# Performance work log

Hardware: AMD Instinct MI355X
Metric: run time of the kernel (lower is better)

Reference implementation:

```python
import jax, jax.numpy as jnp
import numpy as np

N, E, H, C, D_EDGE, G = 50000, 800000, 4, 64, 16, 64
NEG_SLOPE = 0.2  # PyG GATConv default negative_slope
EPS = 1e-5       # GraphNorm eps


def setup_inputs() -> dict:
    key = jax.random.key(0)
    ks = jax.random.split(key, 10)
    node = jax.random.normal(ks[0], (N, C), jnp.float32)
    edge_index = jax.random.randint(ks[1], (2, E), 0, N, dtype=jnp.int32)
    edge_attr = jax.random.normal(ks[2], (E, D_EDGE), jnp.float32)
    batch_ptr = jnp.sort(jax.random.randint(ks[3], (N,), 0, G, dtype=jnp.int32))
    s = 1.0 / np.sqrt(C)
    W = jax.random.normal(ks[4], (C, H * C), jnp.float32) * s
    W_edge = jax.random.normal(ks[5], (D_EDGE, H * C), jnp.float32) / np.sqrt(D_EDGE)
    att_src = jax.random.normal(ks[6], (H, C), jnp.float32) * s
    att_dst = jax.random.normal(ks[7], (H, C), jnp.float32) * s
    att_edge = jax.random.normal(ks[8], (H, C), jnp.float32) * s
    bias = jnp.zeros((C,), jnp.float32)
    gn_weight = jnp.ones((C,), jnp.float32)
    gn_bias = jnp.zeros((C,), jnp.float32)
    gn_scale = jnp.ones((C,), jnp.float32)  # GraphNorm mean_scale
    return dict(node=node, edge_index=edge_index, edge_attr=edge_attr,
                batch_ptr=batch_ptr, W=W, W_edge=W_edge, att_src=att_src,
                att_dst=att_dst, att_edge=att_edge, bias=bias,
                gn_weight=gn_weight, gn_bias=gn_bias, gn_scale=gn_scale)


def reference(node, edge_index, edge_attr, batch_ptr, W, W_edge,
              att_src, att_dst, att_edge, bias, gn_weight, gn_bias, gn_scale):
    src, dst = edge_index[0], edge_index[1]
    # shared src/dst projection (PyG GATConv with int in_channels)
    x = (node @ W).reshape(N, H, C)                      # [N,H,C]
    a_src = (x * att_src).sum(-1)                        # [N,H]
    a_dst = (x * att_dst).sum(-1)                        # [N,H]
    xe = (edge_attr @ W_edge).reshape(E, H, C)           # [E,H,C]
    a_edge = (xe * att_edge).sum(-1)                     # [E,H]
    alpha = a_src[src] + a_dst[dst] + a_edge             # [E,H]
    alpha = jax.nn.leaky_relu(alpha, NEG_SLOPE)
    # segment softmax over incoming edges of each dst node
    amax = jax.ops.segment_max(alpha, dst, num_segments=N)
    amax = jnp.where(jnp.isfinite(amax), amax, 0.0)
    ex = jnp.exp(alpha - amax[dst])
    denom = jax.ops.segment_sum(ex, dst, num_segments=N)
    att = ex / (denom[dst] + 1e-16)                      # [E,H]
    # weighted scatter-add of source features
    msg = x[src] * att[:, :, None]                       # [E,H,C]
    out = jax.ops.segment_sum(msg, dst, num_segments=N)  # [N,H,C]
    out = out.mean(axis=1) + bias                        # concat=False -> head mean
    # GraphNorm(out, batch)
    cnt = jnp.maximum(jax.ops.segment_sum(jnp.ones((N,), out.dtype), batch_ptr,
                                          num_segments=G), 1.0)[:, None]
    mean = jax.ops.segment_sum(out, batch_ptr, num_segments=G) / cnt
    o = out - mean[batch_ptr] * gn_scale
    var = jax.ops.segment_sum(o * o, batch_ptr, num_segments=G) / cnt
    o = o / jnp.sqrt(var + EPS)[batch_ptr]
    y = jax.nn.relu(gn_weight * o + gn_bias)
    return (y, att)
```

## Files before the change

kernel.cpp:

```cpp
#include <hip/hip_runtime.h>
#include <math.h>

#define NN 50000
#define EE 800000
#define HH 4
#define CC 64
#define DE 16
#define GG 64
#define HC 256
#define NEG 0.2f
#define EPSV 1e-5f
#define NB 196
#define SB 16

typedef __attribute__((ext_vector_type(8))) short short8;
typedef __attribute__((ext_vector_type(4))) float f32x4;
typedef __attribute__((ext_vector_type(2))) float f32x2;

__device__ __forceinline__ unsigned short f2bf(float f) {
  unsigned int x = __float_as_uint(f);
  unsigned int r = (x + 0x7fff + ((x >> 16) & 1)) >> 16;
  return (unsigned short)r;
}
__device__ __forceinline__ float lrelu(float a) {
  return fmaxf(a, 0.f) + NEG * fminf(a, 0.f);
}

__global__ __launch_bounds__(256) void k_prep(
    const float* __restrict__ W, const float* __restrict__ We,
    const float* __restrict__ ae_, unsigned short* __restrict__ Wbt,
    float* __restrict__ v_edge, int* __restrict__ hist) {
  int b = blockIdx.x, t = threadIdx.x;
  if (b < 64) {
    Wbt[(size_t)t * 64 + b] = f2bf(W[b * HC + (t & 3) * 64 + (t >> 2)]);
  } else if (b == 64) {
    if (t < DE * HH) {
      int d = t >> 2, h = t & 3;
      float s = 0.f;
      for (int c = 0; c < CC; ++c)
        s += We[d * HC + h * CC + c] * ae_[h * CC + c];
      v_edge[t] = s;
    }
  } else {
    int idx = (b - 65) * 256 + t;
    if (idx < NN) hist[idx] = 0;
  }
}

__global__ __launch_bounds__(256) void k_xproj(
    const float* __restrict__ node, const unsigned short* __restrict__ Wbt,
    const float* __restrict__ att_src, const float* __restrict__ att_dst,
    unsigned short* __restrict__ x16, float* __restrict__ a_src,
    float* __restrict__ a_dst, const int* __restrict__ ei,
    int* __restrict__ hist) {
  {
    int e = blockIdx.x * 256 + threadIdx.x;
    atomicAdd(&hist[ei[EE + e]], 1);
  }
  int lane = threadIdx.x & 63;
  int w = threadIdx.x >> 6;
  int m = lane & 15, quad = lane >> 4;
  int m0 = blockIdx.x * 16;
  __shared__ unsigned short xs[16][260];
  const float* arow = node + (size_t)(m0 + m) * CC + quad * 8;
  float4 af0 = *(const float4*)(arow);
  float4 af1 = *(const float4*)(arow + 4);
  float4 af2 = *(const float4*)(arow + 32);
  float4 af3 = *(const float4*)(arow + 36);
  short8 a0 = {(short)f2bf(af0.x), (short)f2bf(af0.y), (short)f2bf(af0.z),
               (short)f2bf(af0.w), (short)f2bf(af1.x), (short)f2bf(af1.y),
               (short)f2bf(af1.z), (short)f2bf(af1.w)};
  short8 a1 = {(short)f2bf(af2.x), (short)f2bf(af2.y), (short)f2bf(af2.z),
               (short)f2bf(af2.w), (short)f2bf(af3.x), (short)f2bf(af3.y),
               (short)f2bf(af3.z), (short)f2bf(af3.w)};
  float sa[4] = {0, 0, 0, 0}, sd[4] = {0, 0, 0, 0};
#pragma unroll
  for (int i = 0; i < 4; ++i) {
    int t = (w * 4 + i) * 16 + m;
    const unsigned short* bp = Wbt + (size_t)t * 64 + quad * 8;
    short8 b0 = *(const short8*)(bp);
    short8 b1 = *(const short8*)(bp + 32);
    f32x4 acc = {0.f, 0.f, 0.f, 0.f};
    acc = __builtin_amdgcn_mfma_f32_16x16x32_bf16(a0, b0, acc, 0, 0, 0);
    acc = __builtin_amdgcn_mfma_f32_16x16x32_bf16(a1, b1, acc, 0, 0, 0);
    float us_t = att_src[(t & 3) * CC + (t >> 2)];
    float ud_t = att_dst[(t & 3) * CC + (t >> 2)];
#pragma unroll
    for (int r = 0; r < 4; ++r) {
      xs[quad * 4 + r][t] = f2bf(acc[r]);
      sa[r] += acc[r] * us_t;
      sd[r] += acc[r] * ud_t;
    }
  }
  __shared__ float lss[4][16][4], lsd[4][16][4];
#pragma unroll
  for (int r = 0; r < 4; ++r) {
    sa[r] += __shfl_xor(sa[r], 4);
    sa[r] += __shfl_xor(sa[r], 8);
    sd[r] += __shfl_xor(sd[r], 4);
    sd[r] += __shfl_xor(sd[r], 8);
  }
  if ((lane & 12) == 0) {
#pragma unroll
    for (int r = 0; r < 4; ++r) {
      lss[w][quad * 4 + r][lane & 3] = sa[r];
      lsd[w][quad * 4 + r][lane & 3] = sd[r];
    }
  }
  __syncthreads();
  int t = threadIdx.x;
  if (t < 64) {
    int row = t >> 2, h = t & 3;
    a_src[(size_t)(m0 + row) * 4 + h] =
        lss[0][row][h] + lss[1][row][h] + lss[2][row][h] + lss[3][row][h];
    a_dst[(size_t)(m0 + row) * 4 + h] =
        lsd[0][row][h] + lsd[1][row][h] + lsd[2][row][h] + lsd[3][row][h];
  }
  {
    int row = t >> 4, seg = t & 15;
    const unsigned short* xr = &xs[0][0] + row * 260 + seg * 16;
    uint2 lo = *(const uint2*)(xr);
    uint2 hi = *(const uint2*)(xr + 4);
    uint4 o;
    o.x = lo.x; o.y = lo.y; o.z = hi.x; o.w = hi.y;
    uint4* xg = (uint4*)(x16 + (size_t)m0 * HC);
    xg[row * 32 + seg * 2] = o;
    uint2 lo2 = *(const uint2*)(xr + 8);
    uint2 hi2 = *(const uint2*)(xr + 12);
    uint4 o2;
    o2.x = lo2.x; o2.y = lo2.y; o2.z = hi2.x; o2.w = hi2.y;
    xg[row * 32 + seg * 2 + 1] = o2;
  }
}

__global__ __launch_bounds__(256) void k_scanA(
    const int* __restrict__ hist, int* __restrict__ bsum) {
  __shared__ int s[256];
  int t = threadIdx.x;
  int idx = blockIdx.x * 256 + t;
  s[t] = (idx < NN) ? hist[idx] : 0;
  __syncthreads();
  for (int d = 128; d; d >>= 1) {
    if (t < d) s[t] += s[t + d];
    __syncthreads();
  }
  if (t == 0) bsum[blockIdx.x] = s[0];
}

__global__ __launch_bounds__(256) void k_scanC(
    const int* __restrict__ hist, const int* __restrict__ bsum,
    int* __restrict__ ptr, int* __restrict__ cursor) {
  __shared__ int sb_[256];
  __shared__ int s[256];
  int t = threadIdx.x;
  sb_[t] = (t < NB) ? bsum[t] : 0;
  __syncthreads();
  for (int d = 1; d < 256; d <<= 1) {
    int u = (t >= d) ? sb_[t - d] : 0;
    __syncthreads();
    sb_[t] += u;
    __syncthreads();
  }
  int boffv = sb_[blockIdx.x] - bsum[blockIdx.x];
  if (blockIdx.x == NB - 1 && t == 0) ptr[NN] = sb_[NB - 1];
  int idx = blockIdx.x * 256 + t;
  int v = (idx < NN) ? hist[idx] : 0;
  s[t] = v;
  __syncthreads();
  for (int d = 1; d < 256; d <<= 1) {
    int u = (t >= d) ? s[t - d] : 0;
    __syncthreads();
    s[t] += u;
    __syncthreads();
  }
  if (idx < NN) {
    int p = boffv + s[t] - v;
    ptr[idx] = p;
    cursor[idx] = p;
  }
}

__global__ __launch_bounds__(256) void k_edge_perm(
    const float* __restrict__ edge_attr, const int* __restrict__ ei,
    const float* __restrict__ a_src, const float* __restrict__ a_dst,
    const float* __restrict__ v_edge, int* __restrict__ cursor,
    uint4* __restrict__ recs, uint2* __restrict__ t_lin) {
  __shared__ float vs[DE * HH];
  int t = threadIdx.x;
  if (t < DE * HH) vs[t] = v_edge[t];
  __syncthreads();
  int e0 = blockIdx.x * 512 + t;
  int e1 = e0 + 256;
  if (e0 >= EE) return;
  bool has1 = (e1 < EE);
  int e1c = has1 ? e1 : e0;
  int sn0 = ei[e0], dn0 = ei[EE + e0];
  int sn1 = ei[e1c], dn1 = ei[EE + e1c];
  float4 as0 = *(const float4*)(a_src + (size_t)sn0 * 4);
  float4 ad0 = *(const float4*)(a_dst + (size_t)dn0 * 4);
  float4 as1 = *(const float4*)(a_src + (size_t)sn1 * 4);
  float4 ad1 = *(const float4*)(a_dst + (size_t)dn1 * 4);
  const float4* ea0 = (const float4*)(edge_attr + (size_t)e0 * DE);
  const float4* ea1 = (const float4*)(edge_attr + (size_t)e1c * DE);
  float ae0[4] = {0, 0, 0, 0}, ae1[4] = {0, 0, 0, 0};
#pragma unroll
  for (int dd = 0; dd < 4; ++dd) {
    float4 ev0 = ea0[dd];
    float4 ev1 = ea1[dd];
    float evs0[4] = {ev0.x, ev0.y, ev0.z, ev0.w};
    float evs1[4] = {ev1.x, ev1.y, ev1.z, ev1.w};
#pragma unroll
    for (int jj = 0; jj < 4; ++jj) {
      int d = dd * 4 + jj;
#pragma unroll
      for (int h = 0; h < 4; ++h) {
        ae0[h] += evs0[jj] * vs[d * 4 + h];
        ae1[h] += evs1[jj] * vs[d * 4 + h];
      }
    }
  }
  float p0 = __expf(lrelu(as0.x + ad0.x + ae0[0]));
  float p1 = __expf(lrelu(as0.y + ad0.y + ae0[1]));
  float p2 = __expf(lrelu(as0.z + ad0.z + ae0[2]));
  float p3 = __expf(lrelu(as0.w + ad0.w + ae0[3]));
  float q0 = __expf(lrelu(as1.x + ad1.x + ae1[0]));
  float q1 = __expf(lrelu(as1.y + ad1.y + ae1[1]));
  float q2 = __expf(lrelu(as1.z + ad1.z + ae1[2]));
  float q3 = __expf(lrelu(as1.w + ad1.w + ae1[3]));
  uint2 tl0, tl1;
  tl0.x = (unsigned int)f2bf(p0) | ((unsigned int)f2bf(p1) << 16);
  tl0.y = (unsigned int)f2bf(p2) | ((unsigned int)f2bf(p3) << 16);
  tl1.x = (unsigned int)f2bf(q0) | ((unsigned int)f2bf(q1) << 16);
  tl1.y = (unsigned int)f2bf(q2) | ((unsigned int)f2bf(q3) << 16);
  t_lin[e0] = tl0;
  if (has1) t_lin[e1] = tl1;
  int pos0 = atomicAdd(&cursor[dn0], 1);
  int pos1 = has1 ? atomicAdd(&cursor[dn1], 1) : 0;
  uint4 rec0;
  rec0.x = tl0.x; rec0.y = tl0.y;
  rec0.z = (unsigned int)sn0 << 9;
  rec0.w = (unsigned int)e0;
  recs[pos0] = rec0;
  if (has1) {
    uint4 rec1;
    rec1.x = tl1.x; rec1.y = tl1.y;
    rec1.z = (unsigned int)sn1 << 9;
    rec1.w = (unsigned int)e1;
    recs[pos1] = rec1;
  }
}

__global__ __launch_bounds__(256) void k_gat(
    const int* __restrict__ ptr, const uint4* __restrict__ recs,
    const unsigned short* __restrict__ x16, float* __restrict__ out_acc,
    float* __restrict__ rinv) {
  int lane = threadIdx.x & 63;
  int w = threadIdx.x >> 6;
  int v = blockIdx.x * 4 + w;
  int start = __builtin_amdgcn_readfirstlane(ptr[v]);
  int end = __builtin_amdgcn_readfirstlane(ptr[v + 1]);
  f32x2 d01 = {0.f, 0.f}, d23 = {0.f, 0.f};
  f32x2 acc01 = {0.f, 0.f}, acc23 = {0.f, 0.f};
  const char* xbase = (const char*)x16;
  unsigned int lane8 = (unsigned int)lane * 8u;
  int j = start;
#pragma unroll 2
  for (; j + 4 <= end; j += 4) {
    uint4 r0 = recs[j];
    uint4 r1 = recs[j + 1];
    uint4 r2 = recs[j + 2];
    uint4 r3 = recs[j + 3];
    uint2 u0 = *(const uint2*)(xbase + (r0.z + lane8));
    uint2 u1 = *(const uint2*)(xbase + (r1.z + lane8));
    uint2 u2 = *(const uint2*)(xbase + (r2.z + lane8));
    uint2 u3 = *(const uint2*)(xbase + (r3.z + lane8));
#define EDGE_STEP(rn, un)                                              \
    {                                                                  \
      f32x2 ta, tb, xa, xb2;                                           \
      ta.x = __uint_as_float(rn.x << 16);                              \
      ta.y = __uint_as_float(rn.x & 0xffff0000u);                      \
      tb.x = __uint_as_float(rn.y << 16);                              \
      tb.y = __uint_as_float(rn.y & 0xffff0000u);                      \
      xa.x = __uint_as_float(un.x << 16);                              \
      xa.y = __uint_as_float(un.x & 0xffff0000u);                      \
      xb2.x = __uint_as_float(un.y << 16);                             \
      xb2.y = __uint_as_float(un.y & 0xffff0000u);                     \
      d01 += ta;                                                       \
      d23 += tb;                                                       \
      acc01 += ta * xa;                                                \
      acc23 += tb * xb2;                                               \
    }
    EDGE_STEP(r0, u0)
    EDGE_STEP(r1, u1)
    EDGE_STEP(r2, u2)
    EDGE_STEP(r3, u3)
  }
  for (; j < end; ++j) {
    uint4 rec = recs[j];
    uint2 u = *(const uint2*)(xbase + (rec.z + lane8));
    EDGE_STEP(rec, u)
  }
#undef EDGE_STEP
  float r0 = 1.f / (d01.x + 1e-16f), r1 = 1.f / (d01.y + 1e-16f);
  float r2 = 1.f / (d23.x + 1e-16f), r3 = 1.f / (d23.y + 1e-16f);
  out_acc[(size_t)v * CC + lane] =
      0.25f * (r0 * acc01.x + r1 * acc01.y + r2 * acc23.x + r3 * acc23.y);
  if (lane == 0)
    *(float4*)(rinv + (size_t)v * 4) = make_float4(r0, r1, r2, r3);
}

__global__ __launch_bounds__(256) void k_post1(
    const int* __restrict__ batch, const float* __restrict__ out_acc,
    const float* __restrict__ bias, float* __restrict__ p1,
    float* __restrict__ p2, const int* __restrict__ ei,
    const uint2* __restrict__ t_lin, const float* __restrict__ rinv,
    float* __restrict__ att_out) {
  int b = blockIdx.x;
  if (b < GG * SB) {
    int g = b / SB, sb = b % SB;
    int lane = threadIdx.x & 63;
    int w = threadIdx.x >> 6;
    int lo = 0, hi = NN;
    while (lo < hi) {
      int mid = (lo + hi) >> 1;
      if (batch[mid] < g) lo = mid + 1; else hi = mid;
    }
    int start = lo;
    hi = NN;
    while (lo < hi) {
      int mid = (lo + hi) >> 1;
      if (batch[mid] < g + 1) lo = mid + 1; else hi = mid;
    }
    int end = lo;
    int cnt = end - start;
    int chunk = (cnt + SB - 1) / SB;
    int c0 = start + sb * chunk;
    int c1 = min(c0 + chunk, end);
    float bv = bias[lane];
    float s1 = 0.f, s2 = 0.f;
    for (int n = c0 + w; n < c1; n += 4) {
      float v = out_acc[(size_t)n * CC + lane] + bv;
      s1 += v;
      s2 += v * v;
    }
    __shared__ float l1[4][64], l2[4][64];
    l1[w][lane] = s1;
    l2[w][lane] = s2;
    __syncthreads();
    if (w == 0) {
      s1 = l1[0][lane] + l1[1][lane] + l1[2][lane] + l1[3][lane];
      s2 = l2[0][lane] + l2[1][lane] + l2[2][lane] + l2[3][lane];
      p1[(size_t)(g * SB + sb) * 64 + lane] = s1;
      p2[(size_t)(g * SB + sb) * 64 + lane] = s2;
    }
  } else {
    int e = (b - GG * SB) * 256 + threadIdx.x;
    if (e >= EE) return;
    uint2 tl = t_lin[e];
    int dn = ei[EE + e];
    float4 r = *(const float4*)(rinv + (size_t)dn * 4);
    float t0 = __uint_as_float(tl.x << 16);
    float t1 = __uint_as_float(tl.x & 0xffff0000u);
    float t2 = __uint_as_float(tl.y << 16);
    float t3 = __uint_as_float(tl.y & 0xffff0000u);
    *(float4*)(att_out + (size_t)e * 4) =
        make_float4(t0 * r.x, t1 * r.y, t2 * r.z, t3 * r.w);
  }
}

__global__ __launch_bounds__(64) void k_statsB(
    const int* __restrict__ batch, const float* __restrict__ p1,
    const float* __restrict__ p2, const float* __restrict__ gns,
    float* __restrict__ mean_s, float* __restrict__ istd) {
  int g = blockIdx.x;
  int lane = threadIdx.x;
  int lo = 0, hi = NN;
  while (lo < hi) {
    int mid = (lo + hi) >> 1;
    if (batch[mid] < g) lo = mid + 1; else hi = mid;
  }
  int start = lo;
  hi = NN;
  while (lo < hi) {
    int mid = (lo + hi) >> 1;
    if (batch[mid] < g + 1) lo = mid + 1; else hi = mid;
  }
  int end = lo;
  float s1 = 0.f, s2 = 0.f;
#pragma unroll
  for (int sb = 0; sb < SB; ++sb) {
    s1 += p1[(size_t)(g * SB + sb) * 64 + lane];
    s2 += p2[(size_t)(g * SB + sb) * 64 + lane];
  }
  float c = fmaxf((float)(end - start), 1.0f);
  float mean = s1 / c;
  float ms = mean * gns[lane];
  float var = s2 / c - 2.f * ms * mean + ms * ms;
  mean_s[g * CC + lane] = ms;
  istd[g * CC + lane] = rsqrtf(var + EPSV);
}

__global__ __launch_bounds__(256) void k_final(
    const int* __restrict__ batch, const float* __restrict__ out_acc,
    const float* __restrict__ bias, const float* __restrict__ mean_s,
    const float* __restrict__ istd, const float* __restrict__ gnw,
    const float* __restrict__ gnb, float* __restrict__ y) {
  int lane = threadIdx.x & 63;
  int n = blockIdx.x * 4 + (threadIdx.x >> 6);
  int g = batch[n];
  float v = out_acc[(size_t)n * CC + lane] + bias[lane];
  float o = (v - mean_s[g * CC + lane]) * istd[g * CC + lane];
  float r = gnw[lane] * o + gnb[lane];
  y[(size_t)n * CC + lane] = fmaxf(r, 0.0f);
}

extern "C" void kernel_launch(void* const* d_in, const int* in_sizes, int n_in,
                              void* d_out, int out_size, void* d_ws, size_t ws_size,
                              hipStream_t stream) {
  const float* node = (const float*)d_in[0];
  const int* ei = (const int*)d_in[1];
  const float* eatt = (const float*)d_in[2];
  const int* batch = (const int*)d_in[3];
  const float* W = (const float*)d_in[4];
  const float* We = (const float*)d_in[5];
  const float* att_src = (const float*)d_in[6];
  const float* att_dst = (const float*)d_in[7];
  const float* att_edge = (const float*)d_in[8];
  const float* bias = (const float*)d_in[9];
  const float* gnw = (const float*)d_in[10];
  const float* gnb = (const float*)d_in[11];
  const float* gns = (const float*)d_in[12];

  float* ws = (float*)d_ws;
  size_t off = 0;
  uint4* recs = (uint4*)(ws + off);  off += (size_t)EE * 4;
  float* a_src = ws + off;    off += (size_t)NN * HH;
  float* a_dst = ws + off;    off += (size_t)NN * HH;
  float* v_edge = ws + off;   off += 64;
  float* mean_s = ws + off;   off += GG * CC;
  float* istd = ws + off;     off += GG * CC;
  float* out_acc = ws + off;  off += (size_t)NN * CC;
  float* rinv = ws + off;     off += (size_t)NN * HH;
  float* p1 = ws + off;       off += (size_t)GG * SB * 64;
  float* p2 = ws + off;       off += (size_t)GG * SB * 64;
  uint2* t_lin = (uint2*)(ws + off);
  off += (size_t)EE * 2;
  unsigned short* x16 = (unsigned short*)(ws + off);
  off += (size_t)NN * HC / 2;
  unsigned short* Wbt = (unsigned short*)(ws + off);
  off += (size_t)CC * HC / 2;
  int* iws = (int*)(ws + off);
  size_t ioff = 0;
  int* hist = iws + ioff;     ioff += NN;
  int* ptr = iws + ioff;      ioff += NN + 1;
  int* cursor = iws + ioff;   ioff += NN;
  int* bsum = iws + ioff;     ioff += NB;

  float* y_out = (float*)d_out;
  float* att_out = (float*)d_out + (size_t)NN * CC;

  k_prep<<<261, 256, 0, stream>>>(W, We, att_edge, Wbt, v_edge, hist);
  k_xproj<<<NN / 16, 256, 0, stream>>>(node, Wbt, att_src, att_dst, x16, a_src,
                                       a_dst, ei, hist);
  k_scanA<<<NB, 256, 0, stream>>>(hist, bsum);
  k_scanC<<<NB, 256, 0, stream>>>(hist, bsum, ptr, cursor);
  k_edge_perm<<<(EE + 511) / 512, 256, 0, stream>>>(eatt, ei, a_src, a_dst,
                                                    v_edge, cursor, recs,
                                                    t_lin);
  k_gat<<<NN / 4, 256, 0, stream>>>(ptr, recs, x16, out_acc, rinv);
  k_post1<<<GG * SB + (EE + 255) / 256, 256, 0, stream>>>(
      batch, out_acc, bias, p1, p2, ei, t_lin, rinv, att_out);
  k_statsB<<<GG, 64, 0, stream>>>(batch, p1, p2, gns, mean_s, istd);
  k_final<<<NN / 4, 256, 0, stream>>>(batch, out_acc, bias, mean_s, istd, gnw,
                                      gnb, y_out);
}
```

Baseline: 293.6 us.

## Merge scan kernels via decoupled lookback and fold GraphNorm stats into final kernel

Replaces the two-pass block scan (reduce, then scan) with a single-pass scan that uses decoupled lookback over per-block flag/value states, cleared in the prep kernel. It removes the separate GraphNorm statistics kernel by having each final-kernel wavefront recompute mean and inverse std from the partial sums, using a per-graph count written by post1. It also moves the cursor atomics earlier in the edge permutation kernel so their latency overlaps with the gathers. The result is two fewer launches, in exchange for a serial spin-wait chain across scan blocks and redundant stats arithmetic per node in the final kernel.

```diff
diff --git a/kernel.cpp b/kernel.cpp
--- a/kernel.cpp
+++ b/kernel.cpp
@@ -12,6 +12,8 @@
 #define EPSV 1e-5f
 #define NB 196
 #define SB 16
+#define FLAG_A (1u << 30)
+#define FLAG_P (2u << 30)
 
 typedef __attribute__((ext_vector_type(8))) short short8;
 typedef __attribute__((ext_vector_type(4))) float f32x4;
@@ -29,7 +31,8 @@
 __global__ __launch_bounds__(256) void k_prep(
     const float* __restrict__ W, const float* __restrict__ We,
     const float* __restrict__ ae_, unsigned short* __restrict__ Wbt,
-    float* __restrict__ v_edge, int* __restrict__ hist) {
+    float* __restrict__ v_edge, int* __restrict__ hist,
+    unsigned int* __restrict__ state) {
   int b = blockIdx.x, t = threadIdx.x;
   if (b < 64) {
     Wbt[(size_t)t * 64 + b] = f2bf(W[b * HC + (t & 3) * 64 + (t >> 2)]);
@@ -41,9 +44,11 @@
         s += We[d * HC + h * CC + c] * ae_[h * CC + c];
       v_edge[t] = s;
     }
-  } else {
+  } else if (b < 261) {
     int idx = (b - 65) * 256 + t;
     if (idx < NN) hist[idx] = 0;
+  } else {
+    if (t < NB) state[t] = 0u;
   }
 }
 
@@ -133,37 +138,13 @@
   }
 }
 
-__global__ __launch_bounds__(256) void k_scanA(
-    const int* __restrict__ hist, int* __restrict__ bsum) {
+__global__ __launch_bounds__(256) void k_scan(
+    const int* __restrict__ hist, unsigned int* __restrict__ state,
+    int* __restrict__ ptr, int* __restrict__ cursor) {
   __shared__ int s[256];
-  int t = threadIdx.x;
-  int idx = blockIdx.x * 256 + t;
-  s[t] = (idx < NN) ? hist[idx] : 0;
-  __syncthreads();
-  for (int d = 128; d; d >>= 1) {
-    if (t < d) s[t] += s[t + d];
-    __syncthreads();
-  }
-  if (t == 0) bsum[blockIdx.x] = s[0];
-}
-
-__global__ __launch_bounds__(256) void k_scanC(
-    const int* __restrict__ hist, const int* __restrict__ bsum,
-    int* __restrict__ ptr, int* __restrict__ cursor) {
-  __shared__ int sb_[256];
-  __shared__ int s[256];
-  int t = threadIdx.x;
-  sb_[t] = (t < NB) ? bsum[t] : 0;
-  __syncthreads();
-  for (int d = 1; d < 256; d <<= 1) {
-    int u = (t >= d) ? sb_[t - d] : 0;
-    __syncthreads();
-    sb_[t] += u;
-    __syncthreads();
-  }
-  int boffv = sb_[blockIdx.x] - bsum[blockIdx.x];
-  if (blockIdx.x == NB - 1 && t == 0) ptr[NN] = sb_[NB - 1];
-  int idx = blockIdx.x * 256 + t;
+  __shared__ int bx_sh;
+  int b = blockIdx.x, t = threadIdx.x;
+  int idx = b * 256 + t;
   int v = (idx < NN) ? hist[idx] : 0;
   s[t] = v;
   __syncthreads();
@@ -173,11 +154,34 @@
     s[t] += u;
     __syncthreads();
   }
+  int total = s[255];
+  if (t == 0) {
+    if (b == 0) {
+      atomicExch(&state[0], FLAG_P | (unsigned)total);
+      bx_sh = 0;
+    } else {
+      atomicExch(&state[b], FLAG_A | (unsigned)total);
+      int excl = 0;
+      int p = b - 1;
+      while (true) {
+        unsigned sv;
+        do { sv = atomicAdd(&state[p], 0u); } while ((sv >> 30) == 0);
+        excl += (int)(sv & 0x3FFFFFFFu);
+        if (sv & FLAG_P) break;
+        --p;
+      }
+      atomicExch(&state[b], FLAG_P | (unsigned)(excl + total));
+      bx_sh = excl;
+    }
+  }
+  __syncthreads();
+  int bx = bx_sh;
   if (idx < NN) {
-    int p = boffv + s[t] - v;
-    ptr[idx] = p;
-    cursor[idx] = p;
-  }
+    int p2 = bx + s[t] - v;
+    ptr[idx] = p2;
+    cursor[idx] = p2;
+  }
+  if (b == NB - 1 && t == 255) ptr[NN] = bx + total;
 }
 
 __global__ __launch_bounds__(256) void k_edge_perm(
@@ -196,6 +200,8 @@
   int e1c = has1 ? e1 : e0;
   int sn0 = ei[e0], dn0 = ei[EE + e0];
   int sn1 = ei[e1c], dn1 = ei[EE + e1c];
+  int pos0 = atomicAdd(&cursor[dn0], 1);
+  int pos1 = has1 ? atomicAdd(&cursor[dn1], 1) : 0;
   float4 as0 = *(const float4*)(a_src + (size_t)sn0 * 4);
   float4 ad0 = *(const float4*)(a_dst + (size_t)dn0 * 4);
   float4 as1 = *(const float4*)(a_src + (size_t)sn1 * 4);
@@ -234,8 +240,6 @@
   tl1.y = (unsigned int)f2bf(q2) | ((unsigned int)f2bf(q3) << 16);
   t_lin[e0] = tl0;
   if (has1) t_lin[e1] = tl1;
-  int pos0 = atomicAdd(&cursor[dn0], 1);
-  int pos1 = has1 ? atomicAdd(&cursor[dn1], 1) : 0;
   uint4 rec0;
   rec0.x = tl0.x; rec0.y = tl0.y;
   rec0.z = (unsigned int)sn0 << 9;
@@ -312,9 +316,9 @@
 __global__ __launch_bounds__(256) void k_post1(
     const int* __restrict__ batch, const float* __restrict__ out_acc,
     const float* __restrict__ bias, float* __restrict__ p1,
-    float* __restrict__ p2, const int* __restrict__ ei,
-    const uint2* __restrict__ t_lin, const float* __restrict__ rinv,
-    float* __restrict__ att_out) {
+    float* __restrict__ p2, int* __restrict__ gcnt,
+    const int* __restrict__ ei, const uint2* __restrict__ t_lin,
+    const float* __restrict__ rinv, float* __restrict__ att_out) {
   int b = blockIdx.x;
   if (b < GG * SB) {
     int g = b / SB, sb = b % SB;
@@ -333,6 +337,7 @@
     }
     int end = lo;
     int cnt = end - start;
+    if (sb == 0 && threadIdx.x == 0) gcnt[g] = cnt;
     int chunk = (cnt + SB - 1) / SB;
     int c0 = start + sb * chunk;
     int c1 = min(c0 + chunk, end);
@@ -368,48 +373,28 @@
   }
 }
 
-__global__ __launch_bounds__(64) void k_statsB(
-    const int* __restrict__ batch, const float* __restrict__ p1,
-    const float* __restrict__ p2, const float* __restrict__ gns,
-    float* __restrict__ mean_s, float* __restrict__ istd) {
-  int g = blockIdx.x;
-  int lane = threadIdx.x;
-  int lo = 0, hi = NN;
-  while (lo < hi) {
-    int mid = (lo + hi) >> 1;
-    if (batch[mid] < g) lo = mid + 1; else hi = mid;
-  }
-  int start = lo;
-  hi = NN;
-  while (lo < hi) {
-    int mid = (lo + hi) >> 1;
-    if (batch[mid] < g + 1) lo = mid + 1; else hi = mid;
-  }
-  int end = lo;
-  float s1 = 0.f, s2 = 0.f;
-#pragma unroll
-  for (int sb = 0; sb < SB; ++sb) {
-    s1 += p1[(size_t)(g * SB + sb) * 64 + lane];
-    s2 += p2[(size_t)(g * SB + sb) * 64 + lane];
-  }
-  float c = fmaxf((float)(end - start), 1.0f);
-  float mean = s1 / c;
-  float ms = mean * gns[lane];
-  float var = s2 / c - 2.f * ms * mean + ms * ms;
-  mean_s[g * CC + lane] = ms;
-  istd[g * CC + lane] = rsqrtf(var + EPSV);
-}
-
 __global__ __launch_bounds__(256) void k_final(
     const int* __restrict__ batch, const float* __restrict__ out_acc,
-    const float* __restrict__ bias, const float* __restrict__ mean_s,
-    const float* __restrict__ istd, const float* __restrict__ gnw,
+    const float* __restrict__ bias, const float* __restrict__ p1,
+    const float* __restrict__ p2, const int* __restrict__ gcnt,
+    const float* __restrict__ gns, const float* __restrict__ gnw,
     const float* __restrict__ gnb, float* __restrict__ y) {
   int lane = threadIdx.x & 63;
   int n = blockIdx.x * 4 + (threadIdx.x >> 6);
   int g = batch[n];
+  float s1 = 0.f, s2 = 0.f;
+#pragma unroll
+  for (int sb = 0; sb < SB; ++sb) {
+    s1 += p1[(size_t)(g * SB + sb) * 64 + lane];
+    s2 += p2[(size_t)(g * SB + sb) * 64 + lane];
+  }
+  float c = fmaxf((float)gcnt[g], 1.0f);
+  float mean = s1 / c;
+  float ms = mean * gns[lane];
+  float var = s2 / c - 2.f * ms * mean + ms * ms;
+  float istd = rsqrtf(var + EPSV);
   float v = out_acc[(size_t)n * CC + lane] + bias[lane];
-  float o = (v - mean_s[g * CC + lane]) * istd[g * CC + lane];
+  float o = (v - ms) * istd;
   float r = gnw[lane] * o + gnb[lane];
   y[(size_t)n * CC + lane] = fmaxf(r, 0.0f);
 }
@@ -437,8 +422,6 @@
   float* a_src = ws + off;    off += (size_t)NN * HH;
   float* a_dst = ws + off;    off += (size_t)NN * HH;
   float* v_edge = ws + off;   off += 64;
-  float* mean_s = ws + off;   off += GG * CC;
-  float* istd = ws + off;     off += GG * CC;
   float* out_acc = ws + off;  off += (size_t)NN * CC;
   float* rinv = ws + off;     off += (size_t)NN * HH;
   float* p1 = ws + off;       off += (size_t)GG * SB * 64;
@@ -454,23 +437,22 @@
   int* hist = iws + ioff;     ioff += NN;
   int* ptr = iws + ioff;      ioff += NN + 1;
   int* cursor = iws + ioff;   ioff += NN;
-  int* bsum = iws + ioff;     ioff += NB;
+  unsigned int* state = (unsigned int*)(iws + ioff); ioff += NB;
+  int* gcnt = iws + ioff;     ioff += GG;
 
   float* y_out = (float*)d_out;
   float* att_out = (float*)d_out + (size_t)NN * CC;
 
-  k_prep<<<261, 256, 0, stream>>>(W, We, att_edge, Wbt, v_edge, hist);
+  k_prep<<<262, 256, 0, stream>>>(W, We, att_edge, Wbt, v_edge, hist, state);
   k_xproj<<<NN / 16, 256, 0, stream>>>(node, Wbt, att_src, att_dst, x16, a_src,
                                        a_dst, ei, hist);
-  k_scanA<<<NB, 256, 0, stream>>>(hist, bsum);
-  k_scanC<<<NB, 256, 0, stream>>>(hist, bsum, ptr, cursor);
+  k_scan<<<NB, 256, 0, stream>>>(hist, state, ptr, cursor);
   k_edge_perm<<<(EE + 511) / 512, 256, 0, stream>>>(eatt, ei, a_src, a_dst,
                                                     v_edge, cursor, recs,
                                                     t_lin);
   k_gat<<<NN / 4, 256, 0, stream>>>(ptr, recs, x16, out_acc, rinv);
   k_post1<<<GG * SB + (EE + 255) / 256, 256, 0, stream>>>(
-      batch, out_acc, bias, p1, p2, ei, t_lin, rinv, att_out);
-  k_statsB<<<GG, 64, 0, stream>>>(batch, p1, p2, gns, mean_s, istd);
-  k_final<<<NN / 4, 256, 0, stream>>>(batch, out_acc, bias, mean_s, istd, gnw,
-                                      gnb, y_out);
-}
+      batch, out_acc, bias, p1, p2, gcnt, ei, t_lin, rinv, att_out);
+  k_final<<<NN / 4, 256, 0, stream>>>(batch, out_acc, bias, p1, p2, gcnt, gns,
+                                      gnw, gnb, y_out);
+}
```

Measured after the change: 317.8 us. 1.08x slower.
